# Kernel optimization log

Measured on AMD Instinct MI355X. Metric: run time of the kernel, lower is better.

The kernel has to match this reference:

```python
import jax, jax.numpy as jnp
import numpy as np

H, DH, M, ITERS = 8, 64, 256, 6   # heads, dim_head, num_landmarks, pinv iters
DIM = H * DH                      # 512
KERNEL = 33                       # residual depthwise conv kernel


def setup_inputs() -> dict:
    key = jax.random.key(0)
    ks = jax.random.split(key, 5)
    b, n = 2, 8192                # n multiple of M -> no divisibility padding
    x = jax.random.normal(ks[0], (b, n, DIM), jnp.float32)
    ln_gamma = jnp.ones((DIM,), jnp.float32)
    ln_beta = jnp.zeros((DIM,), jnp.float32)
    w_qkv = jax.random.normal(ks[1], (DIM, 3 * DIM), jnp.float32) * 0.02
    w_out = jax.random.normal(ks[2], (DIM, DIM), jnp.float32) * 0.02
    b_out = jnp.zeros((DIM,), jnp.float32)
    res_kernel = jax.random.normal(ks[3], (H, 1, KERNEL, 1), jnp.float32) * 0.02
    return {"x": x, "ln_gamma": ln_gamma, "ln_beta": ln_beta, "w_qkv": w_qkv,
            "w_out": w_out, "b_out": b_out, "res_kernel": res_kernel}


def _pinv(a, iters):
    # lucidrains moore_penrose_iter_pinv (Newton-Schulz iteration)
    abs_a = jnp.abs(a)
    scale = abs_a.sum(-1).max() * abs_a.sum(-2).max()
    z = jnp.swapaxes(a, -1, -2) / scale
    I = jnp.eye(a.shape[-1], dtype=a.dtype)
    for _ in range(iters):
        az = a @ z
        z = 0.25 * z @ (13.0 * I - az @ (15.0 * I - az @ (7.0 * I - az)))
    return z


def reference(x, ln_gamma, ln_beta, w_qkv, w_out, b_out, res_kernel):
    b, n, d = x.shape
    # pre-LayerNorm (eps 1e-5)
    mu = jnp.mean(x, -1, keepdims=True)
    var = jnp.var(x, -1, keepdims=True)
    xn = (x - mu) * jax.lax.rsqrt(var + 1e-5) * ln_gamma + ln_beta
    # qkv projection (bias-free)
    q, k, v = jnp.split(xn @ w_qkv, 3, axis=-1)
    to_heads = lambda t: t.reshape(b, n, H, DH).transpose(0, 2, 1, 3)  # b h n d
    q, k, v = to_heads(q), to_heads(k), to_heads(v)
    q = q * (DH ** -0.5)
    # landmarks: mean over groups of l consecutive tokens ('(m l) d -> m d')
    l = n // M
    q_l = q.reshape(b, H, M, l, DH).mean(3)  # b h M d
    k_l = k.reshape(b, H, M, l, DH).mean(3)
    sim1 = jnp.einsum('bhnd,bhmd->bhnm', q, k_l)      # queries vs k-landmarks
    sim2 = jnp.einsum('bhid,bhjd->bhij', q_l, k_l)    # landmarks vs landmarks
    sim3 = jnp.einsum('bhmd,bhnd->bhmn', q_l, k)      # q-landmarks vs keys
    a1 = jax.nn.softmax(sim1, axis=-1)
    a2 = jax.nn.softmax(sim2, axis=-1)
    a3 = jax.nn.softmax(sim3, axis=-1)
    a2_inv = _pinv(a2, ITERS)
    out = (a1 @ a2_inv) @ (a3 @ v)  # b h n d
    # residual depthwise conv over the sequence axis (Conv2d kernel (33,1), groups=H)
    pad = KERNEL // 2
    out = out + jax.lax.conv_general_dilated(
        v, res_kernel, (1, 1), [(pad, pad), (0, 0)],
        dimension_numbers=('NCHW', 'OIHW', 'NCHW'), feature_group_count=H)
    out = out.transpose(0, 2, 1, 3).reshape(b, n, d)
    out = out @ w_out + b_out  # to_out Linear (dropout inactive at eval)
    return x + out             # TransLayer residual
```

## Files before the change

### kernel.cpp

```cpp
#include <hip/hip_runtime.h>
#include <math.h>

#define H_ 8
#define DH_ 64
#define DIM_ 512
#define M_ 256
#define N_ 8192
#define BH_ 16
#define LG_ 32
#define KC_ 33
#define PADC_ 16

typedef __attribute__((ext_vector_type(8))) short bf16x8;
typedef __attribute__((ext_vector_type(4))) short s16x4;
typedef __attribute__((ext_vector_type(4))) float f32x4;

__device__ __forceinline__ short f2bf(float f) {
  unsigned u = __float_as_uint(f);
  unsigned r = (u + 0x7FFF + ((u >> 16) & 1)) >> 16;
  return (short)r;
}
__device__ __forceinline__ float bf2f(short s) {
  return __uint_as_float(((unsigned)(unsigned short)s) << 16);
}

__device__ __forceinline__ void mfma_nt_core(const short* __restrict__ A,
                                             const short* __restrict__ Bt, int K,
                                             int m0, int n0, size_t lda, size_t ldb,
                                             f32x4 acc[4][4], short* As, short* Bs) {
  const int tid = threadIdx.x;
  const int wave = tid >> 6, lane = tid & 63;
  const int wr = (wave >> 1) * 64, wc = (wave & 1) * 64;
  const int mi = lane & 15, quad = lane >> 4;
  for (int k0 = 0; k0 < K; k0 += 32) {
#pragma unroll
    for (int t = 0; t < 2; ++t) {
      const int cbase = (t * 4 + wave) * 64;
      const int chunk = cbase + lane;
      const int row = chunk >> 2, cc = (chunk & 3) * 8;
      __builtin_amdgcn_global_load_lds(
          (const __attribute__((address_space(1))) void*)(A + (size_t)(m0 + row) * lda + k0 + cc),
          (__attribute__((address_space(3))) void*)(As + (size_t)cbase * 8), 16, 0, 0);
      __builtin_amdgcn_global_load_lds(
          (const __attribute__((address_space(1))) void*)(Bt + (size_t)(n0 + row) * ldb + k0 + cc),
          (__attribute__((address_space(3))) void*)(Bs + (size_t)cbase * 8), 16, 0, 0);
    }
    __syncthreads();
    bf16x8 af[4], bf[4];
#pragma unroll
    for (int i = 0; i < 4; ++i)
      af[i] = *(const bf16x8*)&As[(wr + i * 16 + mi) * 32 + quad * 8];
#pragma unroll
    for (int j = 0; j < 4; ++j)
      bf[j] = *(const bf16x8*)&Bs[(wc + j * 16 + mi) * 32 + quad * 8];
#pragma unroll
    for (int i = 0; i < 4; ++i)
#pragma unroll
      for (int j = 0; j < 4; ++j)
        acc[i][j] = __builtin_amdgcn_mfma_f32_16x16x32_bf16(af[i], bf[j], acc[i][j], 0, 0, 0);
    __syncthreads();
  }
}

__global__ __launch_bounds__(256) void qkv_mfma(const short* __restrict__ xnb,
                                                const short* __restrict__ wt,
                                                short* __restrict__ qb, short* __restrict__ kb,
                                                short* __restrict__ vb) {
  __shared__ short As[128 * 32], Bs[128 * 32];
  f32x4 acc[4][4] = {};
  const int m0 = blockIdx.x * 128, n0 = blockIdx.y * 128;
  mfma_nt_core(xnb, wt, DIM_, m0, n0, DIM_, DIM_, acc, As, Bs);
  const int wave = threadIdx.x >> 6, lane = threadIdx.x & 63;
  const int wr = (wave >> 1) * 64, wc = (wave & 1) * 64;
  const int mi = lane & 15, quad = lane >> 4;
  const int which = n0 >> 9;
  short* dst = which == 0 ? qb : which == 1 ? kb : vb;
  const float sc = which == 0 ? 0.125f : 1.0f;
#pragma unroll
  for (int j = 0; j < 4; ++j) {
    const int col = n0 + wc + j * 16 + mi;
    const int h = (col >> 6) & 7, d = col & 63;
#pragma unroll
    for (int i = 0; i < 4; ++i) {
#pragma unroll
      for (int r = 0; r < 4; ++r) {
        const int row = m0 + wr + i * 16 + quad * 4 + r;
        const int b = row >> 13, t = row & (N_ - 1);
        dst[((size_t)(b * H_ + h) * N_ + t) * DH_ + d] = f2bf(acc[i][j][r] * sc);
      }
    }
  }
}

__global__ __launch_bounds__(256) void final_mfma(const short* __restrict__ omb,
                                                  const short* __restrict__ wt,
                                                  const float* __restrict__ x,
                                                  const float* __restrict__ bout,
                                                  float* __restrict__ y) {
  __shared__ short As[128 * 32], Bs[128 * 32];
  f32x4 acc[4][4] = {};
  const int m0 = blockIdx.x * 128, n0 = blockIdx.y * 128;
  mfma_nt_core(omb, wt, DIM_, m0, n0, DIM_, DIM_, acc, As, Bs);
  const int wave = threadIdx.x >> 6, lane = threadIdx.x & 63;
  const int wr = (wave >> 1) * 64, wc = (wave & 1) * 64;
  const int mi = lane & 15, quad = lane >> 4;
#pragma unroll
  for (int j = 0; j < 4; ++j) {
    const int col = n0 + wc + j * 16 + mi;
    const float bo = bout[col];
#pragma unroll
    for (int i = 0; i < 4; ++i) {
#pragma unroll
      for (int r = 0; r < 4; ++r) {
        const int row = m0 + wr + i * 16 + quad * 4 + r;
        y[(size_t)row * DIM_ + col] = acc[i][j][r] + x[(size_t)row * DIM_ + col] + bo;
      }
    }
  }
}

__global__ __launch_bounds__(256) void convt_kernel(const float* __restrict__ in,
                                                    short* __restrict__ out, int K, int N) {
  __shared__ float tile[32][33];
  const int n0 = blockIdx.x * 32, k0 = blockIdx.y * 32;
  const int tx = threadIdx.x & 31, ty = threadIdx.x >> 5;
  for (int r = ty; r < 32; r += 8) tile[r][tx] = in[(size_t)(k0 + r) * N + n0 + tx];
  __syncthreads();
  for (int r = ty; r < 32; r += 8) out[(size_t)(n0 + r) * K + k0 + tx] = f2bf(tile[tx][r]);
}

__global__ __launch_bounds__(256) void vt_kernel(const short* __restrict__ vb,
                                                 short* __restrict__ vtb) {
  __shared__ short tile[32][33];
  const int t0 = blockIdx.x * 32, d0 = blockIdx.y * 32, bh = blockIdx.z;
  const int tx = threadIdx.x & 31, ty = threadIdx.x >> 5;
  for (int r = ty; r < 32; r += 8)
    tile[r][tx] = vb[((size_t)bh * N_ + t0 + r) * DH_ + d0 + tx];
  __syncthreads();
  for (int r = ty; r < 32; r += 8)
    vtb[((size_t)bh * DH_ + d0 + r) * N_ + t0 + tx] = tile[tx][r];
}

__global__ __launch_bounds__(128) void ln_kernel(const float* __restrict__ x,
                                                 const float* __restrict__ gamma,
                                                 const float* __restrict__ beta,
                                                 short* __restrict__ xnb) {
  const int row = blockIdx.x, tid = threadIdx.x;
  const float4 v = ((const float4*)(x + (size_t)row * DIM_))[tid];
  float s = v.x + v.y + v.z + v.w;
  float ss = v.x * v.x + v.y * v.y + v.z * v.z + v.w * v.w;
  __shared__ float r1[128], r2[128];
  r1[tid] = s;
  r2[tid] = ss;
  __syncthreads();
  for (int off = 64; off > 0; off >>= 1) {
    if (tid < off) {
      r1[tid] += r1[tid + off];
      r2[tid] += r2[tid + off];
    }
    __syncthreads();
  }
  const float mu = r1[0] * (1.0f / DIM_);
  const float var = r2[0] * (1.0f / DIM_) - mu * mu;
  const float rs = rsqrtf(var + 1e-5f);
  const float4 g = ((const float4*)gamma)[tid];
  const float4 bb = ((const float4*)beta)[tid];
  s16x4 o = {f2bf((v.x - mu) * rs * g.x + bb.x), f2bf((v.y - mu) * rs * g.y + bb.y),
             f2bf((v.z - mu) * rs * g.z + bb.z), f2bf((v.w - mu) * rs * g.w + bb.w)};
  ((s16x4*)(xnb + (size_t)row * DIM_))[tid] = o;
}

__global__ __launch_bounds__(256) void landmark_kernel(const short* __restrict__ qb,
                                                       const short* __restrict__ kb,
                                                       float* __restrict__ ql,
                                                       float* __restrict__ kl,
                                                       short* __restrict__ qlb,
                                                       short* __restrict__ klb) {
  const int idx = blockIdx.x * 256 + threadIdx.x;
  const int d = idx & (DH_ - 1);
  const int m = (idx >> 6) & (M_ - 1);
  const int bh = idx >> 14;
  const size_t base = ((size_t)bh * N_ + m * LG_) * DH_ + d;
  float sq = 0.f, sk = 0.f;
#pragma unroll 8
  for (int t = 0; t < LG_; ++t) {
    sq += bf2f(qb[base + (size_t)t * DH_]);
    sk += bf2f(kb[base + (size_t)t * DH_]);
  }
  sq *= (1.0f / LG_);
  sk *= (1.0f / LG_);
  ql[idx] = sq;
  kl[idx] = sk;
  qlb[idx] = f2bf(sq);
  klb[idx] = f2bf(sk);
}

__global__ __launch_bounds__(256) void sim2_softmax(const float* __restrict__ ql,
                                                    const float* __restrict__ kl,
                                                    float* __restrict__ a2,
                                                    short* __restrict__ a2b) {
  const int i = blockIdx.x, bh = blockIdx.y, j = threadIdx.x;
  __shared__ float qrow[DH_];
  if (j < DH_) qrow[j] = ql[((size_t)bh * M_ + i) * DH_ + j];
  __syncthreads();
  const float* kr = kl + ((size_t)bh * M_ + j) * DH_;
  float s = 0.f;
#pragma unroll 16
  for (int d = 0; d < DH_; ++d) s += qrow[d] * kr[d];
  __shared__ float red[256];
  red[j] = s;
  __syncthreads();
  for (int off = 128; off > 0; off >>= 1) {
    if (j < off) red[j] = fmaxf(red[j], red[j + off]);
    __syncthreads();
  }
  const float mx = red[0];
  __syncthreads();
  const float e = expf(s - mx);
  red[j] = e;
  __syncthreads();
  for (int off = 128; off > 0; off >>= 1) {
    if (j < off) red[j] += red[j + off];
    __syncthreads();
  }
  const float out = e / red[0];
  a2[((size_t)bh * M_ + i) * M_ + j] = out;
  a2b[((size_t)bh * M_ + i) * M_ + j] = f2bf(out);
}

__global__ __launch_bounds__(256) void colmax_kernel(const float* __restrict__ a2,
                                                     unsigned int* __restrict__ scalebits) {
  const int bh = blockIdx.x, j = threadIdx.x;
  const float* mat = a2 + (size_t)bh * M_ * M_;
  float s = 0.f;
  for (int i = 0; i < M_; ++i) s += fabsf(mat[i * M_ + j]);
  __shared__ float red[256];
  red[j] = s;
  __syncthreads();
  for (int off = 128; off > 0; off >>= 1) {
    if (j < off) red[j] = fmaxf(red[j], red[j + off]);
    __syncthreads();
  }
  if (j == 0) atomicMax(scalebits, __float_as_uint(red[0]));
}

__global__ __launch_bounds__(256) void transpose_scale(const float* __restrict__ a2,
                                                       short* __restrict__ z0b,
                                                       const unsigned int* __restrict__ scalebits) {
  const float inv = 1.0f / __uint_as_float(*scalebits);
  const int idx = blockIdx.x * 256 + threadIdx.x;
  const int j = idx & (M_ - 1), i = (idx >> 8) & (M_ - 1), bh = idx >> 16;
  z0b[idx] = f2bf(a2[((size_t)bh * M_ + j) * M_ + i] * inv);
}

__device__ __forceinline__ void ns_core(const short* __restrict__ A, const short* __restrict__ B,
                                        int m0, int n0, short* As, short* Bs, f32x4 acc[4]) {
  const int tid = threadIdx.x, wave = tid >> 6, lane = tid & 63;
  const int mi = lane & 15, quad = lane >> 4;
  const int arow = tid >> 2, acol = (tid & 3) * 8;
  const int bkk = tid & 31, g = tid >> 5;
  for (int k0 = 0; k0 < M_; k0 += 32) {
    __builtin_amdgcn_global_load_lds(
        (const __attribute__((address_space(1))) void*)(A + (size_t)(m0 + arow) * M_ + k0 + acol),
        (__attribute__((address_space(3))) void*)(As + (size_t)wave * 512), 16, 0, 0);
    const bf16x8 bv = *(const bf16x8*)(B + (size_t)(k0 + bkk) * M_ + n0 + g * 8);
#pragma unroll
    for (int e = 0; e < 8; ++e) Bs[(g * 8 + e) * 44 + bkk] = bv[e];
    __syncthreads();
    const bf16x8 af = *(const bf16x8*)&As[(wave * 16 + mi) * 32 + quad * 8];
#pragma unroll
    for (int j = 0; j < 4; ++j) {
      union { bf16x8 v; s16x4 h[2]; } bfr;
      const short* bp = &Bs[(j * 16 + mi) * 44 + quad * 8];
      bfr.h[0] = *(const s16x4*)bp;
      bfr.h[1] = *(const s16x4*)(bp + 4);
      acc[j] = __builtin_amdgcn_mfma_f32_16x16x32_bf16(af, bfr.v, acc[j], 0, 0, 0);
    }
    __syncthreads();
  }
}

__global__ __launch_bounds__(256) void ns_gemm0(const short* __restrict__ A,
                                                const short* __restrict__ B,
                                                short* __restrict__ C) {
  __shared__ short As[64 * 32], Bs[64 * 44];
  const int m0 = (blockIdx.x >> 2) * 64, n0 = (blockIdx.x & 3) * 64;
  const size_t mo = (size_t)blockIdx.y * (M_ * M_);
  f32x4 acc[4] = {};
  ns_core(A + mo, B + mo, m0, n0, As, Bs, acc);
  const int wave = threadIdx.x >> 6, lane = threadIdx.x & 63;
  const int mi = lane & 15, quad = lane >> 4;
#pragma unroll
  for (int j = 0; j < 4; ++j)
#pragma unroll
    for (int r = 0; r < 4; ++r) {
      const int row = m0 + wave * 16 + quad * 4 + r, col = n0 + j * 16 + mi;
      C[mo + (size_t)row * M_ + col] = f2bf(acc[j][r]);
    }
}

__global__ __launch_bounds__(256) void ns_stageA(const short* __restrict__ z,
                                                 const short* __restrict__ y,
                                                 short* __restrict__ p1,
                                                 short* __restrict__ y2,
                                                 short* __restrict__ w) {
  __shared__ short As[64 * 32], Bs[64 * 44];
  const int m0 = (blockIdx.x >> 2) * 64, n0 = (blockIdx.x & 3) * 64;
  const int sel = blockIdx.y & 1;
  const size_t mo = (size_t)(blockIdx.y >> 1) * (M_ * M_);
  f32x4 acc[4] = {};
  ns_core((sel ? y : z) + mo, y + mo, m0, n0, As, Bs, acc);
  const int wave = threadIdx.x >> 6, lane = threadIdx.x & 63;
  const int mi = lane & 15, quad = lane >> 4;
#pragma unroll
  for (int j = 0; j < 4; ++j)
#pragma unroll
    for (int r = 0; r < 4; ++r) {
      const int row = m0 + wave * 16 + quad * 4 + r, col = n0 + j * 16 + mi;
      const size_t idx = mo + (size_t)row * M_ + col;
      if (sel) {
        y2[idx] = f2bf(acc[j][r]);
        w[idx] = f2bf(1.75f * bf2f(y[idx]) - 0.25f * acc[j][r]);
      } else {
        p1[idx] = f2bf(acc[j][r]);
      }
    }
}

__global__ __launch_bounds__(256) void ns_stageB(const short* __restrict__ p1,
                                                 const short* __restrict__ y2,
                                                 const short* __restrict__ w,
                                                 const short* __restrict__ z,
                                                 const short* __restrict__ y,
                                                 short* __restrict__ zo,
                                                 short* __restrict__ yo,
                                                 float* __restrict__ zf, int zonly) {
  __shared__ short As[64 * 32], Bs[64 * 44];
  const int m0 = (blockIdx.x >> 2) * 64, n0 = (blockIdx.x & 3) * 64;
  const int sel = zonly ? 0 : (blockIdx.y & 1);
  const size_t mo = (size_t)(zonly ? blockIdx.y : (blockIdx.y >> 1)) * (M_ * M_);
  f32x4 acc[4] = {};
  ns_core((sel ? y2 : p1) + mo, w + mo, m0, n0, As, Bs, acc);
  const int wave = threadIdx.x >> 6, lane = threadIdx.x & 63;
  const int mi = lane & 15, quad = lane >> 4;
#pragma unroll
  for (int j = 0; j < 4; ++j)
#pragma unroll
    for (int r = 0; r < 4; ++r) {
      const int row = m0 + wave * 16 + quad * 4 + r, col = n0 + j * 16 + mi;
      const size_t idx = mo + (size_t)row * M_ + col;
      if (sel) {
        yo[idx] = f2bf(3.25f * bf2f(y[idx]) - 3.75f * bf2f(y2[idx]) + acc[j][r]);
      } else {
        const float v = 3.25f * bf2f(z[idx]) - 3.75f * bf2f(p1[idx]) + acc[j][r];
        zo[idx] = f2bf(v);
        if (zf) zf[idx] = v;
      }
    }
}

__device__ __forceinline__ void mm_step(float (*As)[68], float (*Bs)[68],
                                        int tr, int tc, float acc[4][4]) {
#pragma unroll
  for (int kk = 0; kk < 16; ++kk) {
    const float4 a4 = *(const float4*)&As[kk][tr * 4];
    const float4 b4 = *(const float4*)&Bs[kk][tc * 4];
    const float a[4] = {a4.x, a4.y, a4.z, a4.w};
    const float b[4] = {b4.x, b4.y, b4.z, b4.w};
#pragma unroll
    for (int i = 0; i < 4; ++i)
#pragma unroll
      for (int j = 0; j < 4; ++j) acc[i][j] = fmaf(a[i], b[j], acc[i][j]);
  }
}

__device__ __forceinline__ void load_a_tile(const float* A, int lda, int m0, int k0,
                                            int tid, float (*As)[68]) {
  const int r = tid >> 2, kq = tid & 3;
  const float4 a4 = *(const float4*)(A + (size_t)(m0 + r) * lda + k0 + kq * 4);
  As[kq * 4 + 0][r] = a4.x;
  As[kq * 4 + 1][r] = a4.y;
  As[kq * 4 + 2][r] = a4.z;
  As[kq * 4 + 3][r] = a4.w;
}

__device__ __forceinline__ void load_b_nn(const float* B, int ldb, int k0, int n0,
                                          int tid, float (*Bs)[68]) {
  const int kr = tid >> 4, c4 = tid & 15;
  const float4 b4 = *(const float4*)(B + (size_t)(k0 + kr) * ldb + n0 + c4 * 4);
  *(float4*)&Bs[kr][c4 * 4] = b4;
}

__global__ __launch_bounds__(256) void gemm_nn64(const float* __restrict__ A, int lda,
                                                 long long strideA,
                                                 const float* __restrict__ B, long long strideB,
                                                 float* __restrict__ C, long long strideC,
                                                 int kchunk) {
  const int bz = blockIdx.z;
  A += (size_t)bz * strideA;
  B += (size_t)bz * strideB;
  C += (size_t)bz * strideC;
  const int m0 = blockIdx.x * 64;
  const int tid = threadIdx.x, tr = tid >> 4, tc = tid & 15;
  __shared__ float As[16][68], Bs[16][68];
  float acc[4][4] = {};
  for (int k0 = 0; k0 < kchunk; k0 += 16) {
    load_a_tile(A, lda, m0, k0, tid, As);
    load_b_nn(B, DH_, k0, 0, tid, Bs);
    __syncthreads();
    mm_step(As, Bs, tr, tc, acc);
    __syncthreads();
  }
#pragma unroll
  for (int i = 0; i < 4; ++i) {
    const int row = m0 + tr * 4 + i;
    *(float4*)(C + (size_t)row * DH_ + tc * 4) =
        make_float4(acc[i][0], acc[i][1], acc[i][2], acc[i][3]);
  }
}

__global__ __launch_bounds__(256) void a3_flash(const short* __restrict__ qlb,
                                                const short* __restrict__ kb,
                                                const short* __restrict__ vtb,
                                                float* __restrict__ Opart,
                                                float* __restrict__ mpart,
                                                float* __restrict__ lpart) {
  const int chunk = blockIdx.x, rt = blockIdx.y, bh = blockIdx.z;
  __shared__ short qs[64 * 80], ks[64 * 80], ps[64 * 80];
  const int tid = threadIdx.x, wave = tid >> 6, lane = tid & 63;
  const int mi = lane & 15, quad = lane >> 4;
#pragma unroll
  for (int i = 0; i < 2; ++i) {
    const int c = tid * 2 + i, row = c >> 3, col = (c & 7) * 8;
    *(bf16x8*)&qs[row * 80 + col] =
        *(const bf16x8*)(qlb + ((size_t)bh * M_ + rt * 64 + row) * DH_ + col);
  }
  __syncthreads();
  const bf16x8 aq0 = *(const bf16x8*)&qs[(wave * 16 + mi) * 80 + quad * 8];
  const bf16x8 aq1 = *(const bf16x8*)&qs[(wave * 16 + mi) * 80 + 32 + quad * 8];
  float m[4] = {-INFINITY, -INFINITY, -INFINITY, -INFINITY};
  float l[4] = {0.f, 0.f, 0.f, 0.f};
  f32x4 o[4] = {};
  for (int t = 0; t < 16; ++t) {
    const int n0 = chunk * 1024 + t * 64;
#pragma unroll
    for (int i = 0; i < 2; ++i) {
      const int c = tid * 2 + i, row = c >> 3, col = (c & 7) * 8;
      *(bf16x8*)&ks[row * 80 + col] =
          *(const bf16x8*)(kb + ((size_t)bh * N_ + n0 + row) * DH_ + col);
    }
    __syncthreads();
    f32x4 s[4];
#pragma unroll
    for (int j = 0; j < 4; ++j) {
      const bf16x8 b0 = *(const bf16x8*)&ks[(j * 16 + mi) * 80 + quad * 8];
      const bf16x8 b1 = *(const bf16x8*)&ks[(j * 16 + mi) * 80 + 32 + quad * 8];
      f32x4 z = {0.f, 0.f, 0.f, 0.f};
      z = __builtin_amdgcn_mfma_f32_16x16x32_bf16(aq0, b0, z, 0, 0, 0);
      s[j] = __builtin_amdgcn_mfma_f32_16x16x32_bf16(aq1, b1, z, 0, 0, 0);
    }
    float alpha[4];
#pragma unroll
    for (int r = 0; r < 4; ++r) {
      float v = fmaxf(fmaxf(s[0][r], s[1][r]), fmaxf(s[2][r], s[3][r]));
      v = fmaxf(v, __shfl_xor(v, 1, 64));
      v = fmaxf(v, __shfl_xor(v, 2, 64));
      v = fmaxf(v, __shfl_xor(v, 4, 64));
      v = fmaxf(v, __shfl_xor(v, 8, 64));
      const float mnew = fmaxf(m[r], v);
      alpha[r] = __expf(m[r] - mnew);
      m[r] = mnew;
    }
    float rs[4] = {0.f, 0.f, 0.f, 0.f};
#pragma unroll
    for (int j = 0; j < 4; ++j)
#pragma unroll
      for (int r = 0; r < 4; ++r) {
        const float p = __expf(s[j][r] - m[r]);
        rs[r] += p;
        ps[(wave * 16 + quad * 4 + r) * 80 + j * 16 + mi] = f2bf(p);
      }
#pragma unroll
    for (int r = 0; r < 4; ++r) {
      float v = rs[r];
      v += __shfl_xor(v, 1, 64);
      v += __shfl_xor(v, 2, 64);
      v += __shfl_xor(v, 4, 64);
      v += __shfl_xor(v, 8, 64);
      l[r] = l[r] * alpha[r] + v;
#pragma unroll
      for (int j = 0; j < 4; ++j) o[j][r] *= alpha[r];
    }
    __syncthreads();
    const bf16x8 ap0 = *(const bf16x8*)&ps[(wave * 16 + mi) * 80 + quad * 8];
    const bf16x8 ap1 = *(const bf16x8*)&ps[(wave * 16 + mi) * 80 + 32 + quad * 8];
#pragma unroll
    for (int j = 0; j < 4; ++j) {
      const short* vp = vtb + ((size_t)bh * DH_ + j * 16 + mi) * N_ + n0;
      const bf16x8 b0 = *(const bf16x8*)(vp + quad * 8);
      const bf16x8 b1 = *(const bf16x8*)(vp + 32 + quad * 8);
      o[j] = __builtin_amdgcn_mfma_f32_16x16x32_bf16(ap0, b0, o[j], 0, 0, 0);
      o[j] = __builtin_amdgcn_mfma_f32_16x16x32_bf16(ap1, b1, o[j], 0, 0, 0);
    }
    __syncthreads();
  }
  const int p2 = bh * 4 + rt;
  float* Ob = Opart + ((size_t)chunk * 64 + p2) * 4096;
#pragma unroll
  for (int j = 0; j < 4; ++j)
#pragma unroll
    for (int r = 0; r < 4; ++r)
      Ob[(wave * 16 + quad * 4 + r) * 64 + j * 16 + mi] = o[j][r];
  if (mi == 0) {
#pragma unroll
    for (int r = 0; r < 4; ++r) {
      mpart[((size_t)chunk * 64 + p2) * 64 + wave * 16 + quad * 4 + r] = m[r];
      lpart[((size_t)chunk * 64 + p2) * 64 + wave * 16 + quad * 4 + r] = l[r];
    }
  }
}

__global__ __launch_bounds__(256) void a3_combine(const float* __restrict__ Opart,
                                                  const float* __restrict__ mpart,
                                                  const float* __restrict__ lpart,
                                                  float* __restrict__ a3v) {
  const int p2 = blockIdx.x;
  const int bh = p2 >> 2, rt = p2 & 3;
  __shared__ float wgt[8][64];
  const int tid = threadIdx.x;
  if (tid < 64) {
    float mg = -INFINITY;
    for (int c = 0; c < 8; ++c) mg = fmaxf(mg, mpart[((size_t)c * 64 + p2) * 64 + tid]);
    float e[8], lg = 0.f;
    for (int c = 0; c < 8; ++c) {
      e[c] = __expf(mpart[((size_t)c * 64 + p2) * 64 + tid] - mg);
      lg += lpart[((size_t)c * 64 + p2) * 64 + tid] * e[c];
    }
    const float inv = 1.f / lg;
    for (int c = 0; c < 8; ++c) wgt[c][tid] = e[c] * inv;
  }
  __syncthreads();
  for (int i = tid; i < 4096; i += 256) {
    const int row = i >> 6, d = i & 63;
    float s = 0.f;
    for (int c = 0; c < 8; ++c) s += Opart[((size_t)c * 64 + p2) * 4096 + i] * wgt[c][row];
    a3v[((size_t)bh * M_ + rt * 64 + row) * DH_ + d] = s;
  }
}

__global__ __launch_bounds__(256) void w2t_kernel(const float* __restrict__ w2,
                                                  short* __restrict__ w2tb) {
  const int bh = blockIdx.x, tid = threadIdx.x;
  for (int i = tid; i < M_ * DH_; i += 256) {
    const int r = i >> 6, d = i & 63;
    w2tb[((size_t)bh * DH_ + d) * M_ + r] = f2bf(w2[(size_t)bh * M_ * DH_ + i]);
  }
}

__global__ __launch_bounds__(256) void a1_conv(const short* __restrict__ qb,
                                               const short* __restrict__ klb,
                                               const short* __restrict__ w2tb,
                                               const short* __restrict__ vtb,
                                               const float* __restrict__ rk,
                                               short* __restrict__ omb) {
  __shared__ __align__(16) char smem[35328];
  short* kls = (short*)smem;
  short* vwin = (short*)smem;
  short* band = (short*)(smem + 14848);
  short* ps = (short*)(smem + 17408);
  const int bh = blockIdx.y, t0 = blockIdx.x * 64;
  const int b = bh >> 3, h = bh & 7;
  const int tid = threadIdx.x, wave = tid >> 6, lane = tid & 63;
  const int mi = lane & 15, quad = lane >> 4;

  const short* qrow = qb + ((size_t)bh * N_ + t0 + wave * 16 + mi) * DH_;
  const bf16x8 aq0 = *(const bf16x8*)(qrow + quad * 8);
  const bf16x8 aq1 = *(const bf16x8*)(qrow + 32 + quad * 8);

  f32x4 s[16] = {};
#pragma unroll
  for (int kc = 0; kc < 2; ++kc) {
    if (kc) __syncthreads();
#pragma unroll
    for (int i = 0; i < 4; ++i) {
      const int cb = i * 256 + wave * 64;
      const int c = cb + lane;
      const int row = c >> 2, cc = (c & 3) * 8;
      __builtin_amdgcn_global_load_lds(
          (const __attribute__((address_space(1))) void*)(klb + ((size_t)bh * M_ + row) * DH_ +
                                                          kc * 32 + cc),
          (__attribute__((address_space(3))) void*)(kls + (size_t)cb * 8), 16, 0, 0);
    }
    __syncthreads();
    const bf16x8 aq = kc ? aq1 : aq0;
#pragma unroll
    for (int f = 0; f < 16; ++f) {
      const bf16x8 bf = *(const bf16x8*)&kls[(f * 16 + mi) * 32 + quad * 8];
      s[f] = __builtin_amdgcn_mfma_f32_16x16x32_bf16(aq, bf, s[f], 0, 0, 0);
    }
  }
  float inv[4];
#pragma unroll
  for (int r = 0; r < 4; ++r) {
    float v = s[0][r];
#pragma unroll
    for (int f = 1; f < 16; ++f) v = fmaxf(v, s[f][r]);
    v = fmaxf(v, __shfl_xor(v, 1, 64));
    v = fmaxf(v, __shfl_xor(v, 2, 64));
    v = fmaxf(v, __shfl_xor(v, 4, 64));
    v = fmaxf(v, __shfl_xor(v, 8, 64));
    float sum = 0.f;
#pragma unroll
    for (int f = 0; f < 16; ++f) {
      const float p = __expf(s[f][r] - v);
      s[f][r] = p;
      sum += p;
    }
    sum += __shfl_xor(sum, 1, 64);
    sum += __shfl_xor(sum, 2, 64);
    sum += __shfl_xor(sum, 4, 64);
    sum += __shfl_xor(sum, 8, 64);
    inv[r] = 1.f / sum;
  }
  __syncthreads();

#pragma unroll
  for (int f = 0; f < 8; ++f)
#pragma unroll
    for (int r = 0; r < 4; ++r)
      ps[(wave * 16 + quad * 4 + r) * 140 + f * 16 + mi] = f2bf(s[f][r] * inv[r]);
  {
    const int d = tid & 63, cg0 = tid >> 6;
    const short* vrow = vtb + ((size_t)bh * DH_ + d) * N_;
    for (int ch = cg0; ch < 14; ch += 4) {
      const int tbase = t0 - 16 + ch * 8;
      bf16x8 vv;
      if (tbase >= 0 && tbase + 8 <= N_) {
        vv = *(const bf16x8*)(vrow + tbase);
      } else {
#pragma unroll
        for (int e = 0; e < 8; ++e) {
          const int tt = tbase + e;
          vv[e] = (tt >= 0 && tt < N_) ? vrow[tt] : (short)0;
        }
      }
      *(bf16x8*)&vwin[d * 116 + ch * 8] = vv;
    }
  }
#pragma unroll
  for (int i = 0; i < 4; ++i) {
    const int idx = tid + i * 256;
    const int r = idx >> 6, c = idx & 63, u = c - r;
    band[r * 68 + c] = (u >= 0 && u < KC_) ? f2bf(rk[h * KC_ + u]) : (short)0;
  }
  __syncthreads();

  f32x4 o[4] = {};
#pragma unroll
  for (int k0 = 0; k0 < 4; ++k0) {
    union { bf16x8 v; s16x4 hh[2]; } ap;
    const short* pp = &ps[(wave * 16 + mi) * 140 + k0 * 32 + quad * 8];
    ap.hh[0] = *(const s16x4*)pp;
    ap.hh[1] = *(const s16x4*)(pp + 4);
#pragma unroll
    for (int j = 0; j < 4; ++j) {
      const bf16x8 bw =
          *(const bf16x8*)(w2tb + ((size_t)bh * DH_ + j * 16 + mi) * M_ + k0 * 32 + quad * 8);
      o[j] = __builtin_amdgcn_mfma_f32_16x16x32_bf16(ap.v, bw, o[j], 0, 0, 0);
    }
  }
  __syncthreads();
#pragma unroll
  for (int f = 8; f < 16; ++f)
#pragma unroll
    for (int r = 0; r < 4; ++r)
      ps[(wave * 16 + quad * 4 + r) * 140 + (f - 8) * 16 + mi] = f2bf(s[f][r] * inv[r]);
  __syncthreads();
#pragma unroll
  for (int k0 = 0; k0 < 4; ++k0) {
    union { bf16x8 v; s16x4 hh[2]; } ap;
    const short* pp = &ps[(wave * 16 + mi) * 140 + k0 * 32 + quad * 8];
    ap.hh[0] = *(const s16x4*)pp;
    ap.hh[1] = *(const s16x4*)(pp + 4);
#pragma unroll
    for (int j = 0; j < 4; ++j) {
      const bf16x8 bw = *(const bf16x8*)(w2tb + ((size_t)bh * DH_ + j * 16 + mi) * M_ +
                                         (k0 + 4) * 32 + quad * 8);
      o[j] = __builtin_amdgcn_mfma_f32_16x16x32_bf16(ap.v, bw, o[j], 0, 0, 0);
    }
  }
#pragma unroll
  for (int ks = 0; ks < 2; ++ks) {
    union { bf16x8 v; s16x4 hh[2]; } ab;
    const short* bp = &band[mi * 68 + ks * 32 + quad * 8];
    ab.hh[0] = *(const s16x4*)bp;
    ab.hh[1] = *(const s16x4*)(bp + 4);
#pragma unroll
    for (int j = 0; j < 4; ++j) {
      union { bf16x8 v; s16x4 hh[2]; } bv;
      const short* vp = &vwin[(j * 16 + mi) * 116 + wave * 16 + ks * 32 + quad * 8];
      bv.hh[0] = *(const s16x4*)vp;
      bv.hh[1] = *(const s16x4*)(vp + 4);
      o[j] = __builtin_amdgcn_mfma_f32_16x16x32_bf16(ab.v, bv.v, o[j], 0, 0, 0);
    }
  }
#pragma unroll
  for (int j = 0; j < 4; ++j) {
    const int d = j * 16 + mi;
#pragma unroll
    for (int r = 0; r < 4; ++r) {
      const int t = t0 + wave * 16 + quad * 4 + r;
      omb[((size_t)(b * N_ + t)) * DIM_ + h * DH_ + d] = f2bf(o[j][r]);
    }
  }
}

extern "C" void kernel_launch(void* const* d_in, const int* in_sizes, int n_in,
                              void* d_out, int out_size, void* d_ws, size_t ws_size,
                              hipStream_t stream) {
  (void)in_sizes; (void)n_in; (void)out_size;
  const float* x = (const float*)d_in[0];
  const float* gamma = (const float*)d_in[1];
  const float* beta = (const float*)d_in[2];
  const float* wqkv = (const float*)d_in[3];
  const float* wout = (const float*)d_in[4];
  const float* bout = (const float*)d_in[5];
  const float* rk = (const float*)d_in[6];
  float* y = (float*)d_out;
  float* ws = (float*)d_ws;

  size_t o = 0;
  short* xnb = (short*)(ws + o);   o += (size_t)2 * N_ * DIM_ / 2;
  short* wqkvt = (short*)(ws + o); o += (size_t)3 * DIM_ * DIM_ / 2;
  short* woutt = (short*)(ws + o); o += (size_t)DIM_ * DIM_ / 2;
  short* qb = (short*)(ws + o);    o += (size_t)BH_ * N_ * DH_ / 2;
  short* kb = (short*)(ws + o);    o += (size_t)BH_ * N_ * DH_ / 2;
  short* vb = (short*)(ws + o);    o += (size_t)BH_ * N_ * DH_ / 2;
  short* vtb = (short*)(ws + o);   o += (size_t)BH_ * N_ * DH_ / 2;
  float* ql = ws + o;  o += (size_t)BH_ * M_ * DH_;
  float* kl = ws + o;  o += (size_t)BH_ * M_ * DH_;
  short* qlb = (short*)(ws + o); o += (size_t)BH_ * M_ * DH_ / 2;
  short* klb = (short*)(ws + o); o += (size_t)BH_ * M_ * DH_ / 2;
  float* a2 = ws + o;  o += (size_t)BH_ * M_ * M_;
  float* z0f = ws + o; o += (size_t)BH_ * M_ * M_;
  short* a2b = (short*)(ws + o); o += (size_t)BH_ * M_ * M_ / 2;
  short* zb0 = (short*)(ws + o); o += (size_t)BH_ * M_ * M_ / 2;
  short* zb1 = (short*)(ws + o); o += (size_t)BH_ * M_ * M_ / 2;
  short* yb0 = (short*)(ws + o); o += (size_t)BH_ * M_ * M_ / 2;
  short* yb1 = (short*)(ws + o); o += (size_t)BH_ * M_ * M_ / 2;
  short* p1b = (short*)(ws + o); o += (size_t)BH_ * M_ * M_ / 2;
  short* y2b = (short*)(ws + o); o += (size_t)BH_ * M_ * M_ / 2;
  short* wb  = (short*)(ws + o); o += (size_t)BH_ * M_ * M_ / 2;
  float* Opart = ws + o; o += (size_t)8 * 64 * 4096;
  float* mpart = ws + o; o += (size_t)8 * 64 * 64;
  float* lpart = ws + o; o += (size_t)8 * 64 * 64;
  float* a3v = ws + o; o += (size_t)BH_ * M_ * DH_;
  float* w2 = ws + o;  o += (size_t)BH_ * M_ * DH_;
  short* w2tb = (short*)(ws + o); o += (size_t)BH_ * M_ * DH_ / 2;
  short* omb = (short*)(ws + o);  o += (size_t)2 * N_ * DIM_ / 2;
  unsigned int* scalebits = (unsigned int*)(ws + o); o += 16;
  if (ws_size < o * sizeof(float)) return;

  (void)hipMemsetAsync(scalebits, 0, 64, stream);
  ln_kernel<<<2 * N_, 128, 0, stream>>>(x, gamma, beta, xnb);
  convt_kernel<<<dim3(3 * DIM_ / 32, DIM_ / 32), 256, 0, stream>>>(wqkv, wqkvt, DIM_, 3 * DIM_);
  convt_kernel<<<dim3(DIM_ / 32, DIM_ / 32), 256, 0, stream>>>(wout, woutt, DIM_, DIM_);
  qkv_mfma<<<dim3(2 * N_ / 128, 3 * DIM_ / 128), 256, 0, stream>>>(xnb, wqkvt, qb, kb, vb);
  vt_kernel<<<dim3(N_ / 32, 2, BH_), 256, 0, stream>>>(vb, vtb);

  landmark_kernel<<<BH_ * M_ * DH_ / 256, 256, 0, stream>>>(qb, kb, ql, kl, qlb, klb);
  sim2_softmax<<<dim3(M_, BH_), 256, 0, stream>>>(ql, kl, a2, a2b);
  colmax_kernel<<<BH_, 256, 0, stream>>>(a2, scalebits);
  transpose_scale<<<BH_ * M_ * M_ / 256, 256, 0, stream>>>(a2, zb0, scalebits);

  a3_flash<<<dim3(8, 4, BH_), 256, 0, stream>>>(qlb, kb, vtb, Opart, mpart, lpart);
  a3_combine<<<64, 256, 0, stream>>>(Opart, mpart, lpart, a3v);

  ns_gemm0<<<dim3(16, BH_), 256, 0, stream>>>(a2b, zb0, yb0);
  short* zc = zb0; short* zn = zb1; short* yc = yb0; short* yn = yb1;
  for (int it = 0; it < 6; ++it) {
    const int last = (it == 5);
    ns_stageA<<<dim3(16, 2 * BH_), 256, 0, stream>>>(zc, yc, p1b, y2b, wb);
    ns_stageB<<<dim3(16, last ? BH_ : 2 * BH_), 256, 0, stream>>>(
        p1b, y2b, wb, zc, yc, zn, yn, last ? z0f : nullptr, last);
    short* t;
    t = zc; zc = zn; zn = t;
    t = yc; yc = yn; yn = t;
  }

  gemm_nn64<<<dim3(M_ / 64, 1, BH_), 256, 0, stream>>>(
      z0f, M_, (long long)M_ * M_, a3v, (long long)M_ * DH_, w2, (long long)M_ * DH_, M_);
  w2t_kernel<<<BH_, 256, 0, stream>>>(w2, w2tb);

  a1_conv<<<dim3(N_ / 64, BH_), 256, 0, stream>>>(qb, klb, w2tb, vtb, rk, omb);

  final_mfma<<<dim3(2 * N_ / 128, DIM_ / 128), 256, 0, stream>>>(omb, woutt, x, bout, y);
}
```

Measured before the change: 504.8 us.

## Shrink a1_conv LDS footprint with swizzled key tiles and remap NS GEMM blocks

Restructures a1_conv so the landmark keys load in two row halves with an XOR-swizzled LDS layout. The probability tile, key buffer and value window now share one LDS region, which cuts shared memory from about 35KB to 20KB, and launch_bounds asks for 5 blocks per CU to raise occupancy. The band matrix is built up front and the P·W2 matmul is interleaved per half. Separately, the Newton-Schulz GEMM kernels remap block indices so consecutive blocks spread across matrices, aiming for better cache and XCD distribution. The added barriers and register pressure from the occupancy hint could offset the gains.

After: 474.9 us. -5.9%, faster.

```diff
diff --git a/kernel.cpp b/kernel.cpp
--- a/kernel.cpp
+++ b/kernel.cpp
@@ -280,12 +280,19 @@
   }
 }
 
+__device__ __forceinline__ int ns_remap() {
+  const int lin = blockIdx.y * 16 + blockIdx.x;
+  return (lin & 7) * (gridDim.y << 1) + (lin >> 3);
+}
+
 __global__ __launch_bounds__(256) void ns_gemm0(const short* __restrict__ A,
                                                 const short* __restrict__ B,
                                                 short* __restrict__ C) {
   __shared__ short As[64 * 32], Bs[64 * 44];
-  const int m0 = (blockIdx.x >> 2) * 64, n0 = (blockIdx.x & 3) * 64;
-  const size_t mo = (size_t)blockIdx.y * (M_ * M_);
+  const int id = ns_remap();
+  const int bx = id & 15, by = id >> 4;
+  const int m0 = (bx >> 2) * 64, n0 = (bx & 3) * 64;
+  const size_t mo = (size_t)by * (M_ * M_);
   f32x4 acc[4] = {};
   ns_core(A + mo, B + mo, m0, n0, As, Bs, acc);
   const int wave = threadIdx.x >> 6, lane = threadIdx.x & 63;
@@ -305,9 +312,11 @@
                                                  short* __restrict__ y2,
                                                  short* __restrict__ w) {
   __shared__ short As[64 * 32], Bs[64 * 44];
-  const int m0 = (blockIdx.x >> 2) * 64, n0 = (blockIdx.x & 3) * 64;
-  const int sel = blockIdx.y & 1;
-  const size_t mo = (size_t)(blockIdx.y >> 1) * (M_ * M_);
+  const int id = ns_remap();
+  const int bx = id & 15, by = id >> 4;
+  const int m0 = (bx >> 2) * 64, n0 = (bx & 3) * 64;
+  const int sel = by & 1;
+  const size_t mo = (size_t)(by >> 1) * (M_ * M_);
   f32x4 acc[4] = {};
   ns_core((sel ? y : z) + mo, y + mo, m0, n0, As, Bs, acc);
   const int wave = threadIdx.x >> 6, lane = threadIdx.x & 63;
@@ -336,9 +345,11 @@
                                                  short* __restrict__ yo,
                                                  float* __restrict__ zf, int zonly) {
   __shared__ short As[64 * 32], Bs[64 * 44];
-  const int m0 = (blockIdx.x >> 2) * 64, n0 = (blockIdx.x & 3) * 64;
-  const int sel = zonly ? 0 : (blockIdx.y & 1);
-  const size_t mo = (size_t)(zonly ? blockIdx.y : (blockIdx.y >> 1)) * (M_ * M_);
+  const int id = ns_remap();
+  const int bx = id & 15, by = id >> 4;
+  const int m0 = (bx >> 2) * 64, n0 = (bx & 3) * 64;
+  const int sel = zonly ? 0 : (by & 1);
+  const size_t mo = (size_t)(zonly ? by : (by >> 1)) * (M_ * M_);
   f32x4 acc[4] = {};
   ns_core((sel ? y2 : p1) + mo, w + mo, m0, n0, As, Bs, acc);
   const int wave = threadIdx.x >> 6, lane = threadIdx.x & 63;
@@ -557,17 +568,17 @@
   }
 }
 
-__global__ __launch_bounds__(256) void a1_conv(const short* __restrict__ qb,
-                                               const short* __restrict__ klb,
-                                               const short* __restrict__ w2tb,
-                                               const short* __restrict__ vtb,
-                                               const float* __restrict__ rk,
-                                               short* __restrict__ omb) {
-  __shared__ __align__(16) char smem[35328];
+__global__ __launch_bounds__(256, 5) void a1_conv(const short* __restrict__ qb,
+                                                  const short* __restrict__ klb,
+                                                  const short* __restrict__ w2tb,
+                                                  const short* __restrict__ vtb,
+                                                  const float* __restrict__ rk,
+                                                  short* __restrict__ omb) {
+  __shared__ __align__(16) char smem[20096];
   short* kls = (short*)smem;
+  short* ps = (short*)smem;
   short* vwin = (short*)smem;
-  short* band = (short*)(smem + 14848);
-  short* ps = (short*)(smem + 17408);
+  short* band = (short*)(smem + 17920);
   const int bh = blockIdx.y, t0 = blockIdx.x * 64;
   const int b = bh >> 3, h = bh & 7;
   const int tid = threadIdx.x, wave = tid >> 6, lane = tid & 63;
@@ -577,26 +588,35 @@
   const bf16x8 aq0 = *(const bf16x8*)(qrow + quad * 8);
   const bf16x8 aq1 = *(const bf16x8*)(qrow + 32 + quad * 8);
 
+#pragma unroll
+  for (int i = 0; i < 4; ++i) {
+    const int idx = tid + i * 256;
+    const int r = idx >> 6, c = idx & 63, u = c - r;
+    band[r * 68 + c] = (u >= 0 && u < KC_) ? f2bf(rk[h * KC_ + u]) : (short)0;
+  }
+
   f32x4 s[16] = {};
 #pragma unroll
-  for (int kc = 0; kc < 2; ++kc) {
-    if (kc) __syncthreads();
+  for (int half = 0; half < 2; ++half) {
+    if (half) __syncthreads();
 #pragma unroll
     for (int i = 0; i < 4; ++i) {
       const int cb = i * 256 + wave * 64;
       const int c = cb + lane;
-      const int row = c >> 2, cc = (c & 3) * 8;
+      const int row = c >> 3, cc = c & 7;
       __builtin_amdgcn_global_load_lds(
-          (const __attribute__((address_space(1))) void*)(klb + ((size_t)bh * M_ + row) * DH_ +
-                                                          kc * 32 + cc),
+          (const __attribute__((address_space(1))) void*)(
+              klb + ((size_t)bh * M_ + half * 128 + row) * DH_ + (cc ^ (row & 7)) * 8),
           (__attribute__((address_space(3))) void*)(kls + (size_t)cb * 8), 16, 0, 0);
     }
     __syncthreads();
-    const bf16x8 aq = kc ? aq1 : aq0;
-#pragma unroll
-    for (int f = 0; f < 16; ++f) {
-      const bf16x8 bf = *(const bf16x8*)&kls[(f * 16 + mi) * 32 + quad * 8];
-      s[f] = __builtin_amdgcn_mfma_f32_16x16x32_bf16(aq, bf, s[f], 0, 0, 0);
+#pragma unroll
+    for (int f = 0; f < 8; ++f) {
+      const int row = f * 16 + mi;
+      const bf16x8 blo = *(const bf16x8*)&kls[row * 64 + ((quad ^ (row & 7)) * 8)];
+      const bf16x8 bhi = *(const bf16x8*)&kls[row * 64 + (((quad + 4) ^ (row & 7)) * 8)];
+      f32x4 z = __builtin_amdgcn_mfma_f32_16x16x32_bf16(aq0, blo, s[half * 8 + f], 0, 0, 0);
+      s[half * 8 + f] = __builtin_amdgcn_mfma_f32_16x16x32_bf16(aq1, bhi, z, 0, 0, 0);
     }
   }
   float inv[4];
@@ -624,11 +644,30 @@
   }
   __syncthreads();
 
-#pragma unroll
-  for (int f = 0; f < 8; ++f)
-#pragma unroll
-    for (int r = 0; r < 4; ++r)
-      ps[(wave * 16 + quad * 4 + r) * 140 + f * 16 + mi] = f2bf(s[f][r] * inv[r]);
+  f32x4 o[4] = {};
+#pragma unroll
+  for (int half = 0; half < 2; ++half) {
+#pragma unroll
+    for (int f = 0; f < 8; ++f)
+#pragma unroll
+      for (int r = 0; r < 4; ++r)
+        ps[(wave * 16 + quad * 4 + r) * 140 + f * 16 + mi] = f2bf(s[half * 8 + f][r] * inv[r]);
+#pragma unroll
+    for (int k0 = 0; k0 < 4; ++k0) {
+      union { bf16x8 v; s16x4 hh[2]; } ap;
+      const short* pp = &ps[(wave * 16 + mi) * 140 + k0 * 32 + quad * 8];
+      ap.hh[0] = *(const s16x4*)pp;
+      ap.hh[1] = *(const s16x4*)(pp + 4);
+#pragma unroll
+      for (int j = 0; j < 4; ++j) {
+        const bf16x8 bw = *(const bf16x8*)(w2tb + ((size_t)bh * DH_ + j * 16 + mi) * M_ +
+                                           (half * 4 + k0) * 32 + quad * 8);
+        o[j] = __builtin_amdgcn_mfma_f32_16x16x32_bf16(ap.v, bw, o[j], 0, 0, 0);
+      }
+    }
+  }
+  __syncthreads();
+
   {
     const int d = tid & 63, cg0 = tid >> 6;
     const short* vrow = vtb + ((size_t)bh * DH_ + d) * N_;
@@ -647,48 +686,8 @@
       *(bf16x8*)&vwin[d * 116 + ch * 8] = vv;
     }
   }
-#pragma unroll
-  for (int i = 0; i < 4; ++i) {
-    const int idx = tid + i * 256;
-    const int r = idx >> 6, c = idx & 63, u = c - r;
-    band[r * 68 + c] = (u >= 0 && u < KC_) ? f2bf(rk[h * KC_ + u]) : (short)0;
-  }
-  __syncthreads();
-
-  f32x4 o[4] = {};
-#pragma unroll
-  for (int k0 = 0; k0 < 4; ++k0) {
-    union { bf16x8 v; s16x4 hh[2]; } ap;
-    const short* pp = &ps[(wave * 16 + mi) * 140 + k0 * 32 + quad * 8];
-    ap.hh[0] = *(const s16x4*)pp;
-    ap.hh[1] = *(const s16x4*)(pp + 4);
-#pragma unroll
-    for (int j = 0; j < 4; ++j) {
-      const bf16x8 bw =
-          *(const bf16x8*)(w2tb + ((size_t)bh * DH_ + j * 16 + mi) * M_ + k0 * 32 + quad * 8);
-      o[j] = __builtin_amdgcn_mfma_f32_16x16x32_bf16(ap.v, bw, o[j], 0, 0, 0);
-    }
-  }
-  __syncthreads();
-#pragma unroll
-  for (int f = 8; f < 16; ++f)
-#pragma unroll
-    for (int r = 0; r < 4; ++r)
-      ps[(wave * 16 + quad * 4 + r) * 140 + (f - 8) * 16 + mi] = f2bf(s[f][r] * inv[r]);
-  __syncthreads();
-#pragma unroll
-  for (int k0 = 0; k0 < 4; ++k0) {
-    union { bf16x8 v; s16x4 hh[2]; } ap;
-    const short* pp = &ps[(wave * 16 + mi) * 140 + k0 * 32 + quad * 8];
-    ap.hh[0] = *(const s16x4*)pp;
-    ap.hh[1] = *(const s16x4*)(pp + 4);
-#pragma unroll
-    for (int j = 0; j < 4; ++j) {
-      const bf16x8 bw = *(const bf16x8*)(w2tb + ((size_t)bh * DH_ + j * 16 + mi) * M_ +
-                                         (k0 + 4) * 32 + quad * 8);
-      o[j] = __builtin_amdgcn_mfma_f32_16x16x32_bf16(ap.v, bw, o[j], 0, 0, 0);
-    }
-  }
+  __syncthreads();
+
 #pragma unroll
   for (int ks = 0; ks < 2; ++ks) {
     union { bf16x8 v; s16x4 hh[2]; } ab;
```
